# Optimization experiments

Measured on AMD Instinct MI355X. Metric: run time of the kernel, lower is better.

## Reference

```python
import math
import jax, jax.numpy as jnp
import numpy as np

SEQ_LEN = 512
NUM_HEADS = 16
HEAD_DIM = 64  # hidden_size // num_heads
MAX_REL = 127


def _relative_positions_embeddings(length, depth, max_relative_position=MAX_REL):
    """Sinusoidal table gathered by clipped relative distance -> [L, L, depth]."""
    vocab = 2 * max_relative_position + 1
    pos = np.arange(vocab, dtype=np.float64)[:, None]
    i = np.arange(depth // 2, dtype=np.float64)[None, :]
    angle = pos / np.power(10000.0, 2.0 * i / depth)
    table = np.zeros((vocab, depth), dtype=np.float64)
    table[:, 0::2] = np.sin(angle)
    table[:, 1::2] = np.cos(angle)
    r = np.arange(length)
    dist = np.clip(r[None, :] - r[:, None], -max_relative_position, max_relative_position)
    final = dist + max_relative_position  # [L, L] indices into vocab
    return jnp.asarray(table[final], dtype=jnp.float32)  # [L, L, depth]

_REL_EMB = _relative_positions_embeddings(SEQ_LEN, HEAD_DIM)


def setup_inputs() -> dict:
    key = jax.random.key(0)
    ks = jax.random.split(key, 4)
    B, S, H = 8, SEQ_LEN, NUM_HEADS * HEAD_DIM
    scale = 1.0 / math.sqrt(H)
    return {
        "hidden_states": jax.random.normal(ks[0], (B, S, H), dtype=jnp.float32),
        "attention_mask": jnp.zeros((B, 1, 1, S), dtype=jnp.float32),
        "Wq": jax.random.normal(ks[1], (H, H), dtype=jnp.float32) * scale,
        "bq": jnp.zeros((H,), dtype=jnp.float32),
        "Wk": jax.random.normal(ks[2], (H, H), dtype=jnp.float32) * scale,
        "bk": jnp.zeros((H,), dtype=jnp.float32),
        "Wv": jax.random.normal(ks[3], (H, H), dtype=jnp.float32) * scale,
        "bv": jnp.zeros((H,), dtype=jnp.float32),
    }


def reference(hidden_states, attention_mask, Wq, bq, Wk, bk, Wv, bv):
    B, S, _ = hidden_states.shape
    H, D = NUM_HEADS, HEAD_DIM

    def split_heads(x):  # [B,S,H*D] -> [B,H,S,D]
        return x.reshape(B, S, H, D).transpose(0, 2, 1, 3)

    q = split_heads(hidden_states @ Wq.T + bq)
    k = split_heads(hidden_states @ Wk.T + bk)
    v = split_heads(hidden_states @ Wv.T + bv)

    rel = _REL_EMB[:S, :S, :]  # [S, S, D]

    scores = jnp.einsum("bhqd,bhkd->bhqk", q, k)
    scores = scores + jnp.einsum("bhqd,qkd->bhqk", q, rel)
    scores = scores / math.sqrt(D) + attention_mask

    probs = jax.nn.softmax(scores, axis=-1)  # dropout prob = 0.0 (eval)

    ctx = jnp.einsum("bhqk,bhkd->bhqd", probs, v)
    ctx = ctx + jnp.einsum("bhqk,qkd->bhqd", probs, rel)

    context_layer = ctx.transpose(0, 2, 1, 3).reshape(B, S, H * D)
    return context_layer, scores
```

## Files before the change

### kernel.cpp

```cpp
#include <hip/hip_runtime.h>
#include <hip/hip_bf16.h>

typedef __attribute__((ext_vector_type(4))) float f32x4;
typedef __attribute__((ext_vector_type(8))) short bf16x8;

#define NB 8
#define NS 512
#define NH 16
#define ND 64
#define HID 1024
#define NBH (NB*NH)
#define NROWS (NB*NS)

static __device__ __forceinline__ ushort f2bf(float x){
    union{float f; unsigned u;} a; a.f = x;
    unsigned r = a.u + 0x7fffu + ((a.u >> 16) & 1u);
    return (ushort)(r >> 16);
}
static __device__ __forceinline__ float bf2f(ushort x){
    union{unsigned u; float f;} a; a.u = ((unsigned)x) << 16;
    return a.f;
}

static __device__ __forceinline__ void async_copy16(const void* gsrc, void* ldst){
    __builtin_amdgcn_global_load_lds(
        reinterpret_cast<const __attribute__((address_space(1))) unsigned int*>(
            reinterpret_cast<uintptr_t>(gsrc)),
        reinterpret_cast<__attribute__((address_space(3))) unsigned int*>(
            reinterpret_cast<uintptr_t>(ldst)),
        16, 0, 0);
}

__global__ void build_tables(ushort* __restrict__ tab, ushort* __restrict__ tabT){
    int t = blockIdx.x * blockDim.x + threadIdx.x;
    if (t >= 256 * 64) return;
    int p = t >> 6, d = t & 63;
    float val = 0.f;
    if (p < 255){
        int i = d >> 1;
        float angle = (float)p / powf(10000.f, (float)i / 32.f);
        val = (d & 1) ? cosf(angle) : sinf(angle);
    }
    ushort b = f2bf(val);
    tab[p * 64 + d]  = b;
    tabT[d * 256 + p] = b;
}

__global__ void cvt_bf16(const float* __restrict__ src, ushort* __restrict__ dst, int n4){
    int i = blockIdx.x * blockDim.x + threadIdx.x;
    if (i >= n4) return;
    float4 v = reinterpret_cast<const float4*>(src)[i];
    ushort4 o;
    o.x = f2bf(v.x); o.y = f2bf(v.y); o.z = f2bf(v.z); o.w = f2bf(v.w);
    reinterpret_cast<ushort4*>(dst)[i] = o;
}

__global__ void cvt_bf16_w3(const float* __restrict__ w0, const float* __restrict__ w1,
                            const float* __restrict__ w2, ushort* __restrict__ o0,
                            ushort* __restrict__ o1, ushort* __restrict__ o2, int n4){
    int i = blockIdx.x * blockDim.x + threadIdx.x;
    if (i >= n4) return;
    const float* src = blockIdx.y == 0 ? w0 : (blockIdx.y == 1 ? w1 : w2);
    ushort* dst      = blockIdx.y == 0 ? o0 : (blockIdx.y == 1 ? o1 : o2);
    float4 v = reinterpret_cast<const float4*>(src)[i];
    ushort4 o;
    o.x = f2bf(v.x); o.y = f2bf(v.y); o.z = f2bf(v.z); o.w = f2bf(v.w);
    reinterpret_cast<ushort4*>(dst)[i] = o;
}

__global__ __launch_bounds__(256) void proj_gemm_qkv(
    const ushort* __restrict__ X,
    const ushort* __restrict__ Wqp, const ushort* __restrict__ Wkp, const ushort* __restrict__ Wvp,
    const float* __restrict__ bqp, const float* __restrict__ bkp, const float* __restrict__ bvp,
    ushort* __restrict__ outQ, ushort* __restrict__ outK, ushort* __restrict__ outV)
{
    __shared__ ushort lA[128][64];
    __shared__ ushort lB[128][64];
    int sel = blockIdx.x >> 3;
    const ushort* W   = sel == 0 ? Wqp : (sel == 1 ? Wkp : Wvp);
    const float* bias = sel == 0 ? bqp : (sel == 1 ? bkp : bvp);
    ushort* out       = sel == 0 ? outQ : (sel == 1 ? outK : outV);
    int n0 = (blockIdx.x & 7) * 128;
    int m0 = blockIdx.y * 128;
    int tid = threadIdx.x;
    int wave = tid >> 6, lane = tid & 63;
    int wr = (wave >> 1) * 64, wc = (wave & 1) * 64;
    int lrow = lane & 15, g = lane >> 4;

    const int srow = tid >> 3;
    const int gcol = ((tid & 7) ^ (srow & 7)) * 8;
    char* ldsA = (char*)(&lA[0][0]) + wave * 1024;
    char* ldsB = (char*)(&lB[0][0]) + wave * 1024;
    const int sw = lrow & 7;

    f32x4 acc[4][4] = {};

    for (int k0 = 0; k0 < HID; k0 += 64){
        __syncthreads();
        #pragma unroll
        for (int p = 0; p < 4; ++p){
            async_copy16(&X[(size_t)(m0 + srow + p*32) * HID + k0 + gcol], ldsA + p*4096);
            async_copy16(&W[(size_t)(n0 + srow + p*32) * HID + k0 + gcol], ldsB + p*4096);
        }
        __syncthreads();
        #pragma unroll
        for (int ks = 0; ks < 2; ++ks){
            bf16x8 af[4], bfr[4];
            #pragma unroll
            for (int m = 0; m < 4; ++m)
                af[m] = *reinterpret_cast<const bf16x8*>(
                    &lA[wr + m*16 + lrow][(((ks*4 + g) ^ sw)) * 8]);
            #pragma unroll
            for (int n = 0; n < 4; ++n)
                bfr[n] = *reinterpret_cast<const bf16x8*>(
                    &lB[wc + n*16 + lrow][(((ks*4 + g) ^ sw)) * 8]);
            #pragma unroll
            for (int m = 0; m < 4; ++m)
                #pragma unroll
                for (int n = 0; n < 4; ++n)
                    acc[m][n] = __builtin_amdgcn_mfma_f32_16x16x32_bf16(af[m], bfr[n], acc[m][n], 0, 0, 0);
        }
    }

    #pragma unroll
    for (int m = 0; m < 4; ++m){
        #pragma unroll
        for (int n = 0; n < 4; ++n){
            int col = n0 + wc + n*16 + lrow;
            float bv = bias[col];
            int h = col >> 6, d = col & 63;
            #pragma unroll
            for (int r = 0; r < 4; ++r){
                int mg = m0 + wr + m*16 + (lane >> 4)*4 + r;
                int b = mg >> 9, s = mg & 511;
                float val = acc[m][n][r] + bv;
                if (sel != 2)
                    out[(((size_t)(b*NH + h))*NS + s)*ND + d] = f2bf(val);
                else
                    out[(((size_t)(b*NH + h))*ND + d)*NS + s] = f2bf(val);
            }
        }
    }
}

__global__ __launch_bounds__(256, 6) void fused_attn(
    const ushort* __restrict__ Qb, const ushort* __restrict__ Kb,
    const ushort* __restrict__ vT, const ushort* __restrict__ tab,
    const ushort* __restrict__ tabT, const float* __restrict__ mask,
    float* __restrict__ scores, float* __restrict__ ctx)
{
    __shared__ ushort pL[16][512];
    __shared__ ushort qq[16][256];
    __shared__ float  rsum[16][4];
    __shared__ float  rleft[16][4];
    __shared__ float  rright[16][4];
    ushort* pLf = &pL[0][0];
    ushort* qqf = &qq[0][0];
#define SWZ(row, col) ((col) ^ (((row)&7)<<3))

    const int bh = blockIdx.x;
    const int b = bh >> 4, h = bh & 15;
    const int q0 = blockIdx.y * 16;
    const int wave = threadIdx.x >> 6, lane = threadIdx.x & 63;
    const int lrow = lane & 15, g = lane >> 4, lk8 = g * 8;

    const ushort* Qh = Qb + (size_t)bh * NS * ND;
    const ushort* Kh = Kb + (size_t)bh * NS * ND;
    const int q = q0 + lrow;

    bf16x8 qf0 = *reinterpret_cast<const bf16x8*>(&Qh[(size_t)(q0 + lrow)*ND + lk8]);
    bf16x8 qf1 = *reinterpret_cast<const bf16x8*>(&Qh[(size_t)(q0 + lrow)*ND + 32 + lk8]);

    #pragma unroll
    for (int t = 0; t < 4; ++t){
        const ushort* src = &tab[(size_t)(wave*64 + t*16 + lrow)*ND];
        bf16x8 k0v = *reinterpret_cast<const bf16x8*>(&src[lk8]);
        bf16x8 k1v = *reinterpret_cast<const bf16x8*>(&src[32 + lk8]);
        f32x4 at = __builtin_amdgcn_mfma_f32_16x16x32_bf16(k0v, qf0, (f32x4){0.f,0.f,0.f,0.f}, 0, 0, 0);
        at = __builtin_amdgcn_mfma_f32_16x16x32_bf16(k1v, qf1, at, 0, 0, 0);
        ushort4 w;
        w.x = f2bf(at[0]); w.y = f2bf(at[1]); w.z = f2bf(at[2]); w.w = f2bf(at[3]);
        int col = wave*64 + t*16 + g*4;
        *reinterpret_cast<ushort4*>(&qqf[lrow*256 + SWZ(lrow, col)]) = w;
    }
    __syncthreads();

    float st = 0.f, sl = 0.f, sr = 0.f;
    const float* maskb = &mask[b*NS];
    float* srow = &scores[((size_t)bh*NS + q)*NS];
    const ushort* srcK0 = &Kh[(size_t)(wave*128 + lrow)*ND];
    bf16x8 ka = *reinterpret_cast<const bf16x8*>(&srcK0[lk8]);
    bf16x8 kb = *reinterpret_cast<const bf16x8*>(&srcK0[32 + lk8]);
    #pragma unroll
    for (int n = 0; n < 8; ++n){
        bf16x8 ka1, kb1;
        if (n < 7){
            const ushort* s1 = &Kh[(size_t)(wave*128 + (n+1)*16 + lrow)*ND];
            ka1 = *reinterpret_cast<const bf16x8*>(&s1[lk8]);
            kb1 = *reinterpret_cast<const bf16x8*>(&s1[32 + lk8]);
        }
        int kbase = wave*128 + n*16 + g*4;
        f32x4 a = __builtin_amdgcn_mfma_f32_16x16x32_bf16(ka, qf0, (f32x4){0.f,0.f,0.f,0.f}, 0, 0, 0);
        a = __builtin_amdgcn_mfma_f32_16x16x32_bf16(kb, qf1, a, 0, 0, 0);
        float4 mk4 = *reinterpret_cast<const float4*>(&maskb[kbase]);
        float mk[4] = {mk4.x, mk4.y, mk4.z, mk4.w};
        f32x4 sv;
        ushort4 pw;
        #pragma unroll
        for (int r = 0; r < 4; ++r){
            int k = kbase + r;
            int dd = min(127, max(-127, k - q));
            float val = (a[r] + bf2f(qqf[lrow*256 + SWZ(lrow, dd + 127)])) * 0.125f + mk[r];
            sv[r] = val;
            float e = __expf(val);
            st += e;
            if (k <= q - 127) sl += e;
            if (k >= q + 127) sr += e;
            ((ushort*)&pw)[r] = f2bf(e);
        }
        *reinterpret_cast<f32x4*>(&srow[kbase]) = sv;
        *reinterpret_cast<ushort4*>(&pLf[lrow*512 + SWZ(lrow, kbase)]) = pw;
        ka = ka1; kb = kb1;
    }
    st += __shfl_xor(st, 16); st += __shfl_xor(st, 32);
    sl += __shfl_xor(sl, 16); sl += __shfl_xor(sl, 32);
    sr += __shfl_xor(sr, 16); sr += __shfl_xor(sr, 32);
    if (lane < 16){
        rsum[lrow][wave]   = st;
        rleft[lrow][wave]  = sl;
        rright[lrow][wave] = sr;
    }
    __syncthreads();

    if (wave == 0 && lane < 16){
        float SL = rleft[lrow][0] + rleft[lrow][1] + rleft[lrow][2] + rleft[lrow][3];
        float SR = rright[lrow][0] + rright[lrow][1] + rright[lrow][2] + rright[lrow][3];
        qqf[lrow*256 + SWZ(lrow, 0)]   = f2bf(SL);
        qqf[lrow*256 + SWZ(lrow, 254)] = f2bf(SR);
    }
    for (int idx = threadIdx.x; idx < 16*256; idx += 256){
        int row = idx >> 8, j = idx & 255;
        if (j == 0 || j >= 254) continue;
        int col = q0 + row + j - 127;
        qqf[row*256 + SWZ(row, j)] =
            (col >= 0 && col < NS) ? pLf[row*512 + SWZ(row, col)] : (ushort)0;
    }
    __syncthreads();

    const int d = wave*16 + lrow;
    const ushort* vTh = vT + ((size_t)bh*ND + d)*NS;
    const ushort* tTd = tabT + (size_t)d*256;
    f32x4 o0 = (f32x4){0.f,0.f,0.f,0.f};
    f32x4 o1 = (f32x4){0.f,0.f,0.f,0.f};
    __builtin_amdgcn_s_setprio(1);
    #pragma unroll
    for (int k0 = 0; k0 < NS; k0 += 64){
        bf16x8 bv0 = *reinterpret_cast<const bf16x8*>(&vTh[k0 + lk8]);
        bf16x8 pa0 = *reinterpret_cast<const bf16x8*>(&pLf[lrow*512 + SWZ(lrow, k0 + lk8)]);
        o0 = __builtin_amdgcn_mfma_f32_16x16x32_bf16(pa0, bv0, o0, 0, 0, 0);
        bf16x8 bv1 = *reinterpret_cast<const bf16x8*>(&vTh[k0 + 32 + lk8]);
        bf16x8 pa1 = *reinterpret_cast<const bf16x8*>(&pLf[lrow*512 + SWZ(lrow, k0 + 32 + lk8)]);
        o1 = __builtin_amdgcn_mfma_f32_16x16x32_bf16(pa1, bv1, o1, 0, 0, 0);
    }
    #pragma unroll
    for (int k0 = 0; k0 < 256; k0 += 64){
        bf16x8 bv0 = *reinterpret_cast<const bf16x8*>(&tTd[k0 + lk8]);
        bf16x8 pa0 = *reinterpret_cast<const bf16x8*>(&qqf[lrow*256 + SWZ(lrow, k0 + lk8)]);
        o0 = __builtin_amdgcn_mfma_f32_16x16x32_bf16(pa0, bv0, o0, 0, 0, 0);
        bf16x8 bv1 = *reinterpret_cast<const bf16x8*>(&tTd[k0 + 32 + lk8]);
        bf16x8 pa1 = *reinterpret_cast<const bf16x8*>(&qqf[lrow*256 + SWZ(lrow, k0 + 32 + lk8)]);
        o1 = __builtin_amdgcn_mfma_f32_16x16x32_bf16(pa1, bv1, o1, 0, 0, 0);
    }
    __builtin_amdgcn_s_setprio(0);
    #pragma unroll
    for (int r = 0; r < 4; ++r){
        int row = g*4 + r;
        float T = rsum[row][0] + rsum[row][1] + rsum[row][2] + rsum[row][3];
        int qo = q0 + row;
        ctx[((size_t)b*NS + qo)*HID + h*ND + d] = (o0[r] + o1[r]) * (1.f / T);
    }
#undef SWZ
}

extern "C" void kernel_launch(void* const* d_in, const int* in_sizes, int n_in,
                              void* d_out, int out_size, void* d_ws, size_t ws_size,
                              hipStream_t stream)
{
    const float* x    = (const float*)d_in[0];
    const float* mask = (const float*)d_in[1];
    const float* Wq   = (const float*)d_in[2];
    const float* bq   = (const float*)d_in[3];
    const float* Wk   = (const float*)d_in[4];
    const float* bk   = (const float*)d_in[5];
    const float* Wv   = (const float*)d_in[6];
    const float* bv   = (const float*)d_in[7];

    float* out = (float*)d_out;
    float* ctx    = out;
    float* scores = out + (size_t)NB*NS*HID;

    char* ws = (char*)d_ws;
    ushort* x_bf  = (ushort*)ws;  ws += (size_t)NROWS*HID*2;
    ushort* wq_bf = (ushort*)ws;  ws += (size_t)HID*HID*2;
    ushort* wk_bf = (ushort*)ws;  ws += (size_t)HID*HID*2;
    ushort* wv_bf = (ushort*)ws;  ws += (size_t)HID*HID*2;
    ushort* q_bf  = (ushort*)ws;  ws += (size_t)NBH*NS*ND*2;
    ushort* k_bf  = (ushort*)ws;  ws += (size_t)NBH*NS*ND*2;
    ushort* vT_bf = (ushort*)ws;  ws += (size_t)NBH*NS*ND*2;
    ushort* tab   = (ushort*)ws;  ws += 256*64*2;
    ushort* tabT  = (ushort*)ws;  ws += 64*256*2;

    build_tables<<<64, 256, 0, stream>>>(tab, tabT);

    cvt_bf16<<<(NROWS*HID/4 + 255)/256, 256, 0, stream>>>(x, x_bf, NROWS*HID/4);
    cvt_bf16_w3<<<dim3((HID*HID/4 + 255)/256, 3), 256, 0, stream>>>(
        Wq, Wk, Wv, wq_bf, wk_bf, wv_bf, HID*HID/4);

    proj_gemm_qkv<<<dim3(24, 32), 256, 0, stream>>>(
        x_bf, wq_bf, wk_bf, wv_bf, bq, bk, bv, q_bf, k_bf, vT_bf);

    fused_attn<<<dim3(NBH, NS/16), 256, 0, stream>>>(
        q_bf, k_bf, vT_bf, tab, tabT, mask, scores, ctx);
}
```

Measured before the change: 173.6 us.

## Fuse fp32-to-bf16 conversion of inputs and weights into QKV projection GEMM loads

Removes the separate conversion kernels for hidden states and the three weight matrices. The projection GEMM now loads fp32 tiles directly, converts them to bf16 with packed convert instructions, and stores them into LDS. This drops two launches and the bf16 workspace round trip. In exchange, the GEMM reads twice the bytes per tile and re-converts each tile for every block that uses it, and it loses the async global-to-LDS copy path.

Measured after the change: 157.9 us, median of 2. -9.0%, faster.

```diff
diff --git a/kernel.cpp b/kernel.cpp
--- a/kernel.cpp
+++ b/kernel.cpp
@@ -22,13 +22,13 @@
     return a.f;
 }
 
-static __device__ __forceinline__ void async_copy16(const void* gsrc, void* ldst){
-    __builtin_amdgcn_global_load_lds(
-        reinterpret_cast<const __attribute__((address_space(1))) unsigned int*>(
-            reinterpret_cast<uintptr_t>(gsrc)),
-        reinterpret_cast<__attribute__((address_space(3))) unsigned int*>(
-            reinterpret_cast<uintptr_t>(ldst)),
-        16, 0, 0);
+static __device__ __forceinline__ bf16x8 cvt8(const float4 a, const float4 b){
+    union { bf16x8 v; unsigned u[4]; } r;
+    asm volatile("v_cvt_pk_bf16_f32 %0, %1, %2" : "=v"(r.u[0]) : "v"(a.x), "v"(a.y));
+    asm volatile("v_cvt_pk_bf16_f32 %0, %1, %2" : "=v"(r.u[1]) : "v"(a.z), "v"(a.w));
+    asm volatile("v_cvt_pk_bf16_f32 %0, %1, %2" : "=v"(r.u[2]) : "v"(b.x), "v"(b.y));
+    asm volatile("v_cvt_pk_bf16_f32 %0, %1, %2" : "=v"(r.u[3]) : "v"(b.z), "v"(b.w));
+    return r.v;
 }
 
 __global__ void build_tables(ushort* __restrict__ tab, ushort* __restrict__ tabT){
@@ -46,38 +46,16 @@
     tabT[d * 256 + p] = b;
 }
 
-__global__ void cvt_bf16(const float* __restrict__ src, ushort* __restrict__ dst, int n4){
-    int i = blockIdx.x * blockDim.x + threadIdx.x;
-    if (i >= n4) return;
-    float4 v = reinterpret_cast<const float4*>(src)[i];
-    ushort4 o;
-    o.x = f2bf(v.x); o.y = f2bf(v.y); o.z = f2bf(v.z); o.w = f2bf(v.w);
-    reinterpret_cast<ushort4*>(dst)[i] = o;
-}
-
-__global__ void cvt_bf16_w3(const float* __restrict__ w0, const float* __restrict__ w1,
-                            const float* __restrict__ w2, ushort* __restrict__ o0,
-                            ushort* __restrict__ o1, ushort* __restrict__ o2, int n4){
-    int i = blockIdx.x * blockDim.x + threadIdx.x;
-    if (i >= n4) return;
-    const float* src = blockIdx.y == 0 ? w0 : (blockIdx.y == 1 ? w1 : w2);
-    ushort* dst      = blockIdx.y == 0 ? o0 : (blockIdx.y == 1 ? o1 : o2);
-    float4 v = reinterpret_cast<const float4*>(src)[i];
-    ushort4 o;
-    o.x = f2bf(v.x); o.y = f2bf(v.y); o.z = f2bf(v.z); o.w = f2bf(v.w);
-    reinterpret_cast<ushort4*>(dst)[i] = o;
-}
-
 __global__ __launch_bounds__(256) void proj_gemm_qkv(
-    const ushort* __restrict__ X,
-    const ushort* __restrict__ Wqp, const ushort* __restrict__ Wkp, const ushort* __restrict__ Wvp,
+    const float* __restrict__ X,
+    const float* __restrict__ Wqp, const float* __restrict__ Wkp, const float* __restrict__ Wvp,
     const float* __restrict__ bqp, const float* __restrict__ bkp, const float* __restrict__ bvp,
     ushort* __restrict__ outQ, ushort* __restrict__ outK, ushort* __restrict__ outV)
 {
     __shared__ ushort lA[128][64];
     __shared__ ushort lB[128][64];
     int sel = blockIdx.x >> 3;
-    const ushort* W   = sel == 0 ? Wqp : (sel == 1 ? Wkp : Wvp);
+    const float* W    = sel == 0 ? Wqp : (sel == 1 ? Wkp : Wvp);
     const float* bias = sel == 0 ? bqp : (sel == 1 ? bkp : bvp);
     ushort* out       = sel == 0 ? outQ : (sel == 1 ? outK : outV);
     int n0 = (blockIdx.x & 7) * 128;
@@ -89,8 +67,7 @@
 
     const int srow = tid >> 3;
     const int gcol = ((tid & 7) ^ (srow & 7)) * 8;
-    char* ldsA = (char*)(&lA[0][0]) + wave * 1024;
-    char* ldsB = (char*)(&lB[0][0]) + wave * 1024;
+    const int lcol = (tid & 7) * 8;
     const int sw = lrow & 7;
 
     f32x4 acc[4][4] = {};
@@ -99,8 +76,14 @@
         __syncthreads();
         #pragma unroll
         for (int p = 0; p < 4; ++p){
-            async_copy16(&X[(size_t)(m0 + srow + p*32) * HID + k0 + gcol], ldsA + p*4096);
-            async_copy16(&W[(size_t)(n0 + srow + p*32) * HID + k0 + gcol], ldsB + p*4096);
+            const float* xs = &X[(size_t)(m0 + srow + p*32) * HID + k0 + gcol];
+            float4 xa = *reinterpret_cast<const float4*>(xs);
+            float4 xb = *reinterpret_cast<const float4*>(xs + 4);
+            const float* wsrc = &W[(size_t)(n0 + srow + p*32) * HID + k0 + gcol];
+            float4 wa = *reinterpret_cast<const float4*>(wsrc);
+            float4 wb = *reinterpret_cast<const float4*>(wsrc + 4);
+            *reinterpret_cast<bf16x8*>(&lA[srow + p*32][lcol]) = cvt8(xa, xb);
+            *reinterpret_cast<bf16x8*>(&lB[srow + p*32][lcol]) = cvt8(wa, wb);
         }
         __syncthreads();
         #pragma unroll
@@ -300,10 +283,6 @@
     float* scores = out + (size_t)NB*NS*HID;
 
     char* ws = (char*)d_ws;
-    ushort* x_bf  = (ushort*)ws;  ws += (size_t)NROWS*HID*2;
-    ushort* wq_bf = (ushort*)ws;  ws += (size_t)HID*HID*2;
-    ushort* wk_bf = (ushort*)ws;  ws += (size_t)HID*HID*2;
-    ushort* wv_bf = (ushort*)ws;  ws += (size_t)HID*HID*2;
     ushort* q_bf  = (ushort*)ws;  ws += (size_t)NBH*NS*ND*2;
     ushort* k_bf  = (ushort*)ws;  ws += (size_t)NBH*NS*ND*2;
     ushort* vT_bf = (ushort*)ws;  ws += (size_t)NBH*NS*ND*2;
@@ -312,12 +291,8 @@
 
     build_tables<<<64, 256, 0, stream>>>(tab, tabT);
 
-    cvt_bf16<<<(NROWS*HID/4 + 255)/256, 256, 0, stream>>>(x, x_bf, NROWS*HID/4);
-    cvt_bf16_w3<<<dim3((HID*HID/4 + 255)/256, 3), 256, 0, stream>>>(
-        Wq, Wk, Wv, wq_bf, wk_bf, wv_bf, HID*HID/4);
-
     proj_gemm_qkv<<<dim3(24, 32), 256, 0, stream>>>(
-        x_bf, wq_bf, wk_bf, wv_bf, bq, bk, bv, q_bf, k_bf, vT_bf);
+        x, Wq, Wk, Wv, bq, bk, bv, q_bf, k_bf, vT_bf);
 
     fused_attn<<<dim3(NBH, NS/16), 256, 0, stream>>>(
         q_bf, k_bf, vT_bf, tab, tabT, mask, scores, ctx);
```
